# Kernel tuning notes

Measured on AMD Instinct MI355X. Metric: run time of the kernel, lower is better.

The kernel has to match this reference:

```python
import jax, jax.numpy as jnp
import numpy as np

D_MODEL = 1024
NUM_HEADS = 16
HEAD_DIM = D_MODEL // NUM_HEADS


def setup_inputs() -> dict:
    key = jax.random.key(0)
    ks = jax.random.split(key, 9)
    B, S = 2, 2048
    s = 1.0 / np.sqrt(D_MODEL)
    inp = {
        "x": jax.random.normal(ks[0], (B, S, D_MODEL), dtype=jnp.float32),
        "Wq": jax.random.normal(ks[1], (D_MODEL, D_MODEL), dtype=jnp.float32) * s,
        "bq": jnp.zeros((D_MODEL,), dtype=jnp.float32),
        "Wk": jax.random.normal(ks[2], (D_MODEL, D_MODEL), dtype=jnp.float32) * s,
        "bk": jnp.zeros((D_MODEL,), dtype=jnp.float32),
        "Wv": jax.random.normal(ks[3], (D_MODEL, D_MODEL), dtype=jnp.float32) * s,
        "bv": jnp.zeros((D_MODEL,), dtype=jnp.float32),
        "Wo": jax.random.normal(ks[4], (D_MODEL, D_MODEL), dtype=jnp.float32) * s,
        "bo": jnpp if False else jnp.zeros((D_MODEL,), dtype=jnp.float32),
    }
    return inp


def reference(x, Wq, bq, Wk, bk, Wv, bv, Wo, bo):
    B, S, D = x.shape
    H, hd = NUM_HEADS, HEAD_DIM
    # QKV projections (Linear: x @ W^T + b), split into heads -> [B,H,S,hd]
    q = (x @ Wq.T + bq).reshape(B, S, H, hd).transpose(0, 2, 1, 3)
    k = (x @ Wk.T + bk).reshape(B, S, H, hd).transpose(0, 2, 1, 3)
    v = (x @ Wv.T + bv).reshape(B, S, H, hd).transpose(0, 2, 1, 3)
    # scores [B,H,S,S]
    scores = jnp.einsum('bhqd,bhkd->bhqk', q, k) / jnp.sqrt(jnp.float32(hd))
    p = jax.nn.softmax(scores, axis=-1)
    out = jnp.einsum('bhqk,bhkd->bhqd', p, v)  # [B,H,S,hd]
    out = out.transpose(0, 2, 1, 3).reshape(B, S, D)
    return out @ Wo.T + bo
```

## Files before the change

### kernel.cpp

```cpp
#include <hip/hip_runtime.h>
#include <hip/hip_bf16.h>
#include <math.h>

typedef __bf16 bf16;
typedef unsigned short u16;
typedef __bf16 bf16x8 __attribute__((ext_vector_type(8)));
typedef __bf16 bf16x4 __attribute__((ext_vector_type(4)));
typedef short  s16x4  __attribute__((ext_vector_type(4)));
typedef float  f32x4  __attribute__((ext_vector_type(4)));

#define D_MODEL 1024
#define NHEAD   16
#define HD      64
#define BATCH   2
#define SEQ     2048
#define MTOT    (BATCH*SEQ)

#define EXPSCALE 0.18033688011116016f

__device__ __forceinline__ void async16(const void* g, void* l) {
    __builtin_amdgcn_global_load_lds(
        (__attribute__((address_space(1))) unsigned int*)g,
        (__attribute__((address_space(3))) unsigned int*)l,
        16, 0, 0);
}

__device__ __forceinline__ f32x4 mfma16(s16x4 a, s16x4 b, f32x4 c) {
    return __builtin_amdgcn_mfma_f32_16x16x16bf16_1k(a, b, c, 0, 0, 0);
}

__global__ __launch_bounds__(256) void cast_kernel(
    const float* __restrict__ x,
    const float* __restrict__ wq, const float* __restrict__ wk,
    const float* __restrict__ wv, const float* __restrict__ wo,
    bf16* __restrict__ xb, bf16* __restrict__ wqb, bf16* __restrict__ wkb,
    bf16* __restrict__ wvb, bf16* __restrict__ wob)
{
    const int z = blockIdx.y;
    const float* src;
    bf16* dst;
    int n;
    if (z == 0)      { src = x;  dst = xb;  n = MTOT * D_MODEL; }
    else if (z == 1) { src = wq; dst = wqb; n = D_MODEL * D_MODEL; }
    else if (z == 2) { src = wk; dst = wkb; n = D_MODEL * D_MODEL; }
    else if (z == 3) { src = wv; dst = wvb; n = D_MODEL * D_MODEL; }
    else             { src = wo; dst = wob; n = D_MODEL * D_MODEL; }

    int i = (blockIdx.x * 256 + threadIdx.x) * 8;
    if (i >= n) return;
    float4 a = *(const float4*)(src + i);
    float4 b = *(const float4*)(src + i + 4);
    bf16x8 o;
    o[0] = (bf16)a.x; o[1] = (bf16)a.y; o[2] = (bf16)a.z; o[3] = (bf16)a.w;
    o[4] = (bf16)b.x; o[5] = (bf16)b.y; o[6] = (bf16)b.z; o[7] = (bf16)b.w;
    *(bf16x8*)(dst + i) = o;
}

__device__ __forceinline__ void gemm_core(const bf16* __restrict__ A,
                                          const bf16* __restrict__ W,
                                          int m0, int n0,
                                          f32x4 acc[4][4],
                                          u16* lA, u16* lB)
{
    const int tid  = threadIdx.x;
    const int lane = tid & 63;
    const int wave = tid >> 6;
    const int wr   = wave >> 1;
    const int wc   = wave & 1;
    const int fr   = lane & 15;
    const int quad = lane >> 4;

    #pragma unroll
    for (int mi = 0; mi < 4; ++mi)
        #pragma unroll
        for (int ni = 0; ni < 4; ++ni)
            #pragma unroll
            for (int e = 0; e < 4; ++e)
                acc[mi][ni][e] = 0.0f;

    const int row = tid >> 3;
    const int ca  = ((tid & 7) ^ (row & 7)) * 8;
    const bf16* gA[4];
    const bf16* gB[4];
    u16 *sA[4], *sB[4];
    #pragma unroll
    for (int c = 0; c < 4; ++c) {
        int slot = tid + c * 256;
        int r    = row + c * 32;
        gA[c] = A + (size_t)(m0 + r) * 1024 + ca;
        gB[c] = W + (size_t)(n0 + r) * 1024 + ca;
        sA[c] = lA + (size_t)slot * 8;
        sB[c] = lB + (size_t)slot * 8;
    }

    for (int kt = 0; kt < 1024 / 64; ++kt) {
        __syncthreads();
        #pragma unroll
        for (int c = 0; c < 4; ++c) {
            async16(gA[c] + kt * 64, sA[c]);
            async16(gB[c] + kt * 64, sB[c]);
        }
        __syncthreads();

        #pragma unroll
        for (int ks = 0; ks < 2; ++ks) {
            const int sa = ((ks * 4 + quad) ^ (fr & 7)) * 8;
            bf16x8 af[4], bfm[4];
            #pragma unroll
            for (int mi = 0; mi < 4; ++mi)
                af[mi] = *(const bf16x8*)(lA + (wr * 64 + mi * 16 + fr) * 64 + sa);
            #pragma unroll
            for (int ni = 0; ni < 4; ++ni)
                bfm[ni] = *(const bf16x8*)(lB + (wc * 64 + ni * 16 + fr) * 64 + sa);

            #pragma unroll
            for (int mi = 0; mi < 4; ++mi)
                #pragma unroll
                for (int ni = 0; ni < 4; ++ni)
                    acc[mi][ni] = __builtin_amdgcn_mfma_f32_16x16x32_bf16(
                        af[mi], bfm[ni], acc[mi][ni], 0, 0, 0);
        }
    }
}

__global__ __launch_bounds__(256) void qkv_kernel(
    const bf16* __restrict__ x,
    const bf16* __restrict__ Wq, const bf16* __restrict__ Wk, const bf16* __restrict__ Wv,
    const float* __restrict__ bq, const float* __restrict__ bk, const float* __restrict__ bv,
    bf16* __restrict__ Q, bf16* __restrict__ K, bf16* __restrict__ Vt)
{
    __shared__ __align__(16) u16 lA[128 * 64];
    __shared__ __align__(16) u16 lB[128 * 64];

    const int z = blockIdx.z;
    int m0, n0;
    const bf16 *mA, *mB;
    const float* bias;
    if (z == 2) {
        mA = Wv; mB = x; bias = bv;
        m0 = blockIdx.y * 128;
        n0 = blockIdx.x * 128;
    } else {
        mA = x;  mB = (z == 0) ? Wq : Wk; bias = (z == 0) ? bq : bk;
        m0 = blockIdx.x * 128;
        n0 = blockIdx.y * 128;
    }

    f32x4 acc[4][4];
    gemm_core(mA, mB, m0, n0, acc, lA, lB);

    const int lane = threadIdx.x & 63;
    const int wave = threadIdx.x >> 6;
    const int wr = wave >> 1, wc = wave & 1;
    const int col = lane & 15, quad = lane >> 4;

    if (z == 2) {
        #pragma unroll
        for (int mi = 0; mi < 4; ++mi) {
            #pragma unroll
            for (int ni = 0; ni < 4; ++ni) {
                #pragma unroll
                for (int r = 0; r < 4; ++r) {
                    int f = m0 + wr * 64 + mi * 16 + quad * 4 + r;
                    int t = n0 + wc * 64 + ni * 16 + col;
                    float v = acc[mi][ni][r] + bias[f];
                    int b = t >> 11, s = t & 2047;
                    int h = f >> 6,  d = f & 63;
                    Vt[((size_t)(b * NHEAD + h) * HD + d) * SEQ + s] = (bf16)v;
                }
            }
        }
    } else {
        const float qs = (z == 0) ? EXPSCALE : 1.0f;
        bf16* o = (z == 0) ? Q : K;
        #pragma unroll
        for (int mi = 0; mi < 4; ++mi) {
            #pragma unroll
            for (int ni = 0; ni < 4; ++ni) {
                #pragma unroll
                for (int r = 0; r < 4; ++r) {
                    int m = m0 + wr * 64 + mi * 16 + quad * 4 + r;
                    int n = n0 + wc * 64 + ni * 16 + col;
                    float v = (acc[mi][ni][r] + bias[n]) * qs;
                    int b = m >> 11, s = m & 2047;
                    int h = n >> 6,  d = n & 63;
                    o[((size_t)(b * NHEAD + h) * SEQ + s) * HD + d] = (bf16)v;
                }
            }
        }
    }
}

__global__ __launch_bounds__(256, 4) void attn_kernel(
    const bf16* __restrict__ Q, const bf16* __restrict__ K,
    const bf16* __restrict__ Vt, bf16* __restrict__ O)
{
    __shared__ __align__(16) u16 lK[64 * 64];
    __shared__ __align__(16) u16 lV[64 * 64];

    const int tid  = threadIdx.x;
    const int lane = tid & 63;
    const int wave = tid >> 6;
    const int col  = lane & 15;
    const int quad = lane >> 4;
    const int bh   = blockIdx.x;
    const int q0   = blockIdx.y * 64;

    const bf16* Qh = Q  + (size_t)bh * SEQ * HD;
    const bf16* Kh = K  + (size_t)bh * SEQ * HD;
    const bf16* Vh = Vt + (size_t)bh * HD * SEQ;

    bf16x8 qf[2];
    #pragma unroll
    for (int ks = 0; ks < 2; ++ks)
        qf[ks] = *(const bf16x8*)(
            Qh + (size_t)(q0 + wave * 16 + col) * HD + ks * 32 + quad * 8);

    f32x4 acc_o[4];
    #pragma unroll
    for (int nd = 0; nd < 4; ++nd)
        #pragma unroll
        for (int e = 0; e < 4; ++e) acc_o[nd][e] = 0.0f;
    float rs = 0.0f;
    const f32x4 zero4 = {0.0f, 0.0f, 0.0f, 0.0f};

    const int r0 = tid >> 3;
    const int r1 = r0 + 32;
    const int g0 = (((tid & 7) ^ (r0 & 7))) * 8;
    const int g1 = (((tid & 7) ^ (r1 & 7))) * 8;
    const bf16* gK0 = Kh + (size_t)r0 * HD + g0;
    const bf16* gK1 = Kh + (size_t)r1 * HD + g1;
    const bf16* gV0 = Vh + (size_t)r0 * SEQ + g0;
    const bf16* gV1 = Vh + (size_t)r1 * SEQ + g1;
    u16* sK0 = lK + (size_t)tid * 8;
    u16* sK1 = lK + (size_t)(tid + 256) * 8;
    u16* sV0 = lV + (size_t)tid * 8;
    u16* sV1 = lV + (size_t)(tid + 256) * 8;

    for (int jt = 0; jt < SEQ / 64; ++jt) {
        __syncthreads();
        async16(gK0 + (size_t)jt * 64 * HD, sK0);
        async16(gK1 + (size_t)jt * 64 * HD, sK1);
        async16(gV0 + jt * 64, sV0);
        async16(gV1 + jt * 64, sV1);
        __syncthreads();

        f32x4 sc[4];
        #pragma unroll
        for (int nj = 0; nj < 4; ++nj) {
            bf16x8 kf0 = *(const bf16x8*)(
                lK + (nj * 16 + col) * 64 + ((0 + quad) ^ (col & 7)) * 8);
            sc[nj] = __builtin_amdgcn_mfma_f32_16x16x32_bf16(kf0, qf[0], zero4, 0, 0, 0);
        }
        #pragma unroll
        for (int nj = 0; nj < 4; ++nj) {
            bf16x8 kf1 = *(const bf16x8*)(
                lK + (nj * 16 + col) * 64 + ((4 + quad) ^ (col & 7)) * 8);
            sc[nj] = __builtin_amdgcn_mfma_f32_16x16x32_bf16(kf1, qf[1], sc[nj], 0, 0, 0);
        }

        s16x4 pb[4];
        #pragma unroll
        for (int nj = 0; nj < 4; ++nj) {
            float p0 = __builtin_amdgcn_exp2f(sc[nj][0]);
            float p1 = __builtin_amdgcn_exp2f(sc[nj][1]);
            float p2 = __builtin_amdgcn_exp2f(sc[nj][2]);
            float p3 = __builtin_amdgcn_exp2f(sc[nj][3]);
            rs += (p0 + p1) + (p2 + p3);
            bf16x4 t;
            t[0] = (bf16)p0; t[1] = (bf16)p1; t[2] = (bf16)p2; t[3] = (bf16)p3;
            pb[nj] = __builtin_bit_cast(s16x4, t);
        }

        #pragma unroll
        for (int nj = 0; nj < 4; ++nj) {
            #pragma unroll
            for (int nd = 0; nd < 4; ++nd) {
                int row = nd * 16 + col;
                int jb  = (2 * nj + (quad >> 1)) ^ (row & 7);
                s16x4 vb = *(const s16x4*)(lV + row * 64 + jb * 8 + (quad & 1) * 4);
                acc_o[nd] = mfma16(pb[nj], vb, acc_o[nd]);
            }
        }
    }

    const int b = bh >> 4, h = bh & 15;
    float v = rs;
    v += __shfl_xor(v, 16);
    v += __shfl_xor(v, 32);
    float inv = 1.0f / v;
    float invr[4];
    #pragma unroll
    for (int r = 0; r < 4; ++r)
        invr[r] = __shfl(inv, quad * 4 + r);
    #pragma unroll
    for (int nd = 0; nd < 4; ++nd) {
        #pragma unroll
        for (int r = 0; r < 4; ++r) {
            int srow = q0 + wave * 16 + quad * 4 + r;
            int d    = nd * 16 + col;
            float o  = acc_o[nd][r] * invr[r];
            O[((size_t)(b * SEQ + srow)) * D_MODEL + h * HD + d] = (bf16)o;
        }
    }
}

__global__ __launch_bounds__(256) void oproj_kernel(
    const bf16* __restrict__ A, const bf16* __restrict__ Wo,
    const float* __restrict__ bo, float* __restrict__ out)
{
    __shared__ __align__(16) u16 lA[128 * 64];
    __shared__ __align__(16) u16 lB[64 * 64];

    const int m0 = blockIdx.x * 128;
    const int n0 = blockIdx.y * 64;

    const int tid  = threadIdx.x;
    const int lane = tid & 63;
    const int wave = tid >> 6;
    const int wr   = wave >> 1;
    const int wc   = wave & 1;
    const int fr   = lane & 15;
    const int quad = lane >> 4;

    f32x4 acc[4][2];
    #pragma unroll
    for (int mi = 0; mi < 4; ++mi)
        #pragma unroll
        for (int ni = 0; ni < 2; ++ni)
            #pragma unroll
            for (int e = 0; e < 4; ++e)
                acc[mi][ni][e] = 0.0f;

    const int row = tid >> 3;
    const int ca  = ((tid & 7) ^ (row & 7)) * 8;
    const bf16* gA[4];
    u16* sA[4];
    #pragma unroll
    for (int c = 0; c < 4; ++c) {
        int slot = tid + c * 256;
        gA[c] = A + (size_t)(m0 + row + c * 32) * 1024 + ca;
        sA[c] = lA + (size_t)slot * 8;
    }
    const bf16* gB[2];
    u16* sB[2];
    #pragma unroll
    for (int c = 0; c < 2; ++c) {
        int slot = tid + c * 256;
        gB[c] = Wo + (size_t)(n0 + row + c * 32) * 1024 + ca;
        sB[c] = lB + (size_t)slot * 8;
    }

    for (int kt = 0; kt < 1024 / 64; ++kt) {
        __syncthreads();
        #pragma unroll
        for (int c = 0; c < 4; ++c) async16(gA[c] + kt * 64, sA[c]);
        #pragma unroll
        for (int c = 0; c < 2; ++c) async16(gB[c] + kt * 64, sB[c]);
        __syncthreads();

        #pragma unroll
        for (int ks = 0; ks < 2; ++ks) {
            const int sa = ((ks * 4 + quad) ^ (fr & 7)) * 8;
            bf16x8 af[4], bfm[2];
            #pragma unroll
            for (int mi = 0; mi < 4; ++mi)
                af[mi] = *(const bf16x8*)(lA + (wr * 64 + mi * 16 + fr) * 64 + sa);
            #pragma unroll
            for (int ni = 0; ni < 2; ++ni)
                bfm[ni] = *(const bf16x8*)(lB + (wc * 32 + ni * 16 + fr) * 64 + sa);

            #pragma unroll
            for (int mi = 0; mi < 4; ++mi)
                #pragma unroll
                for (int ni = 0; ni < 2; ++ni)
                    acc[mi][ni] = __builtin_amdgcn_mfma_f32_16x16x32_bf16(
                        af[mi], bfm[ni], acc[mi][ni], 0, 0, 0);
        }
    }

    const int col = fr;
    #pragma unroll
    for (int mi = 0; mi < 4; ++mi) {
        #pragma unroll
        for (int ni = 0; ni < 2; ++ni) {
            #pragma unroll
            for (int r = 0; r < 4; ++r) {
                int m = m0 + wr * 64 + mi * 16 + quad * 4 + r;
                int n = n0 + wc * 32 + ni * 16 + col;
                out[(size_t)m * D_MODEL + n] = acc[mi][ni][r] + bo[n];
            }
        }
    }
}

extern "C" void kernel_launch(void* const* d_in, const int* in_sizes, int n_in,
                              void* d_out, int out_size, void* d_ws, size_t ws_size,
                              hipStream_t stream)
{
    const float* x  = (const float*)d_in[0];
    const float* Wq = (const float*)d_in[1];
    const float* bq = (const float*)d_in[2];
    const float* Wk = (const float*)d_in[3];
    const float* bk = (const float*)d_in[4];
    const float* Wv = (const float*)d_in[5];
    const float* bv = (const float*)d_in[6];
    const float* Wo = (const float*)d_in[7];
    const float* bo = (const float*)d_in[8];
    float* out = (float*)d_out;

    char* ws = (char*)d_ws;
    const size_t XSZ = (size_t)MTOT * D_MODEL * sizeof(bf16);
    const size_t WSZ = (size_t)D_MODEL * D_MODEL * sizeof(bf16);
    bf16* wqb = (bf16*)(ws);
    bf16* wkb = (bf16*)(ws + WSZ);
    bf16* wvb = (bf16*)(ws + 2 * WSZ);
    bf16* wob = (bf16*)(ws + 3 * WSZ);
    bf16* xb  = (bf16*)(ws + 4 * WSZ);
    bf16* Qb  = (bf16*)(ws + 4 * WSZ + XSZ);
    bf16* Kb  = (bf16*)(ws + 4 * WSZ + 2 * XSZ);
    bf16* Vt  = (bf16*)(ws + 4 * WSZ + 3 * XSZ);
    bf16* At  = (bf16*)(ws + 4 * WSZ + 4 * XSZ);

    cast_kernel<<<dim3((MTOT * D_MODEL) / (256 * 8), 5), 256, 0, stream>>>(
        x, Wq, Wk, Wv, Wo, xb, wqb, wkb, wvb, wob);

    qkv_kernel<<<dim3(32, 8, 3), 256, 0, stream>>>(
        xb, wqb, wkb, wvb, bq, bk, bv, Qb, Kb, Vt);

    attn_kernel<<<dim3(BATCH * NHEAD, SEQ / 64), 256, 0, stream>>>(Qb, Kb, Vt, At);

    oproj_kernel<<<dim3(MTOT / 128, D_MODEL / 64), 256, 0, stream>>>(At, wob, bo, out);
}
```

Measured before the change: 197.0 us.

## Process two query sub-tiles per wave in attention to reuse K/V tiles

Measured after the change: 192.1 us. 1.03x faster.

```diff
diff --git a/kernel.cpp b/kernel.cpp
--- a/kernel.cpp
+++ b/kernel.cpp
@@ -191,7 +191,7 @@
     }
 }
 
-__global__ __launch_bounds__(256, 4) void attn_kernel(
+__global__ __launch_bounds__(256, 2) void attn_kernel(
     const bf16* __restrict__ Q, const bf16* __restrict__ K,
     const bf16* __restrict__ Vt, bf16* __restrict__ O)
 {
@@ -204,24 +204,28 @@
     const int col  = lane & 15;
     const int quad = lane >> 4;
     const int bh   = blockIdx.x;
-    const int q0   = blockIdx.y * 64;
+    const int q0   = blockIdx.y * 128;
 
     const bf16* Qh = Q  + (size_t)bh * SEQ * HD;
     const bf16* Kh = K  + (size_t)bh * SEQ * HD;
     const bf16* Vh = Vt + (size_t)bh * HD * SEQ;
 
-    bf16x8 qf[2];
-    #pragma unroll
-    for (int ks = 0; ks < 2; ++ks)
-        qf[ks] = *(const bf16x8*)(
-            Qh + (size_t)(q0 + wave * 16 + col) * HD + ks * 32 + quad * 8);
-
-    f32x4 acc_o[4];
-    #pragma unroll
-    for (int nd = 0; nd < 4; ++nd)
-        #pragma unroll
-        for (int e = 0; e < 4; ++e) acc_o[nd][e] = 0.0f;
-    float rs = 0.0f;
+    bf16x8 qf[2][2];
+    #pragma unroll
+    for (int qb = 0; qb < 2; ++qb)
+        #pragma unroll
+        for (int ks = 0; ks < 2; ++ks)
+            qf[qb][ks] = *(const bf16x8*)(
+                Qh + (size_t)(q0 + wave * 32 + qb * 16 + col) * HD + ks * 32 + quad * 8);
+
+    f32x4 acc_o[2][4];
+    #pragma unroll
+    for (int qb = 0; qb < 2; ++qb)
+        #pragma unroll
+        for (int nd = 0; nd < 4; ++nd)
+            #pragma unroll
+            for (int e = 0; e < 4; ++e) acc_o[qb][nd][e] = 0.0f;
+    float rs[2] = {0.0f, 0.0f};
     const f32x4 zero4 = {0.0f, 0.0f, 0.0f, 0.0f};
 
     const int r0 = tid >> 3;
@@ -245,31 +249,36 @@
         async16(gV1 + jt * 64, sV1);
         __syncthreads();
 
-        f32x4 sc[4];
+        f32x4 sc[2][4];
         #pragma unroll
         for (int nj = 0; nj < 4; ++nj) {
             bf16x8 kf0 = *(const bf16x8*)(
                 lK + (nj * 16 + col) * 64 + ((0 + quad) ^ (col & 7)) * 8);
-            sc[nj] = __builtin_amdgcn_mfma_f32_16x16x32_bf16(kf0, qf[0], zero4, 0, 0, 0);
+            sc[0][nj] = __builtin_amdgcn_mfma_f32_16x16x32_bf16(kf0, qf[0][0], zero4, 0, 0, 0);
+            sc[1][nj] = __builtin_amdgcn_mfma_f32_16x16x32_bf16(kf0, qf[1][0], zero4, 0, 0, 0);
         }
         #pragma unroll
         for (int nj = 0; nj < 4; ++nj) {
             bf16x8 kf1 = *(const bf16x8*)(
                 lK + (nj * 16 + col) * 64 + ((4 + quad) ^ (col & 7)) * 8);
-            sc[nj] = __builtin_amdgcn_mfma_f32_16x16x32_bf16(kf1, qf[1], sc[nj], 0, 0, 0);
-        }
-
-        s16x4 pb[4];
-        #pragma unroll
-        for (int nj = 0; nj < 4; ++nj) {
-            float p0 = __builtin_amdgcn_exp2f(sc[nj][0]);
-            float p1 = __builtin_amdgcn_exp2f(sc[nj][1]);
-            float p2 = __builtin_amdgcn_exp2f(sc[nj][2]);
-            float p3 = __builtin_amdgcn_exp2f(sc[nj][3]);
-            rs += (p0 + p1) + (p2 + p3);
-            bf16x4 t;
-            t[0] = (bf16)p0; t[1] = (bf16)p1; t[2] = (bf16)p2; t[3] = (bf16)p3;
-            pb[nj] = __builtin_bit_cast(s16x4, t);
+            sc[0][nj] = __builtin_amdgcn_mfma_f32_16x16x32_bf16(kf1, qf[0][1], sc[0][nj], 0, 0, 0);
+            sc[1][nj] = __builtin_amdgcn_mfma_f32_16x16x32_bf16(kf1, qf[1][1], sc[1][nj], 0, 0, 0);
+        }
+
+        s16x4 pb[2][4];
+        #pragma unroll
+        for (int qb = 0; qb < 2; ++qb) {
+            #pragma unroll
+            for (int nj = 0; nj < 4; ++nj) {
+                float p0 = __builtin_amdgcn_exp2f(sc[qb][nj][0]);
+                float p1 = __builtin_amdgcn_exp2f(sc[qb][nj][1]);
+                float p2 = __builtin_amdgcn_exp2f(sc[qb][nj][2]);
+                float p3 = __builtin_amdgcn_exp2f(sc[qb][nj][3]);
+                rs[qb] += (p0 + p1) + (p2 + p3);
+                bf16x4 t;
+                t[0] = (bf16)p0; t[1] = (bf16)p1; t[2] = (bf16)p2; t[3] = (bf16)p3;
+                pb[qb][nj] = __builtin_bit_cast(s16x4, t);
+            }
         }
 
         #pragma unroll
@@ -279,28 +288,32 @@
                 int row = nd * 16 + col;
                 int jb  = (2 * nj + (quad >> 1)) ^ (row & 7);
                 s16x4 vb = *(const s16x4*)(lV + row * 64 + jb * 8 + (quad & 1) * 4);
-                acc_o[nd] = mfma16(pb[nj], vb, acc_o[nd]);
+                acc_o[0][nd] = mfma16(pb[0][nj], vb, acc_o[0][nd]);
+                acc_o[1][nd] = mfma16(pb[1][nj], vb, acc_o[1][nd]);
             }
         }
     }
 
     const int b = bh >> 4, h = bh & 15;
-    float v = rs;
-    v += __shfl_xor(v, 16);
-    v += __shfl_xor(v, 32);
-    float inv = 1.0f / v;
-    float invr[4];
-    #pragma unroll
-    for (int r = 0; r < 4; ++r)
-        invr[r] = __shfl(inv, quad * 4 + r);
-    #pragma unroll
-    for (int nd = 0; nd < 4; ++nd) {
-        #pragma unroll
-        for (int r = 0; r < 4; ++r) {
-            int srow = q0 + wave * 16 + quad * 4 + r;
-            int d    = nd * 16 + col;
-            float o  = acc_o[nd][r] * invr[r];
-            O[((size_t)(b * SEQ + srow)) * D_MODEL + h * HD + d] = (bf16)o;
+    #pragma unroll
+    for (int qb = 0; qb < 2; ++qb) {
+        float v = rs[qb];
+        v += __shfl_xor(v, 16);
+        v += __shfl_xor(v, 32);
+        float inv = 1.0f / v;
+        float invr[4];
+        #pragma unroll
+        for (int r = 0; r < 4; ++r)
+            invr[r] = __shfl(inv, quad * 4 + r);
+        #pragma unroll
+        for (int nd = 0; nd < 4; ++nd) {
+            #pragma unroll
+            for (int r = 0; r < 4; ++r) {
+                int srow = q0 + wave * 32 + qb * 16 + quad * 4 + r;
+                int d    = nd * 16 + col;
+                float o  = acc_o[qb][nd][r] * invr[r];
+                O[((size_t)(b * SEQ + srow)) * D_MODEL + h * HD + d] = (bf16)o;
+            }
         }
     }
 }
@@ -428,7 +441,7 @@
     qkv_kernel<<<dim3(32, 8, 3), 256, 0, stream>>>(
         xb, wqb, wkb, wvb, bq, bk, bv, Qb, Kb, Vt);
 
-    attn_kernel<<<dim3(BATCH * NHEAD, SEQ / 64), 256, 0, stream>>>(Qb, Kb, Vt, At);
+    attn_kernel<<<dim3(BATCH * NHEAD, SEQ / 128), 256, 0, stream>>>(Qb, Kb, Vt, At);
 
     oproj_kernel<<<dim3(MTOT / 128, D_MODEL / 64), 256, 0, stream>>>(At, wob, bo, out);
 }
```
